# Optimization experiments

Measured on AMD Instinct MI355X. Metric: run time of the kernel, lower is better.

Reference implementation:

```python
import jax, jax.numpy as jnp
import numpy as np
from jax.scipy.ndimage import map_coordinates

IMG = 256
N_ANG = 50
BATCH = 4
N_CNN = 32
IN_CH = 2


def _circle_mask(S):
    c = (S - 1) / 2.0
    yy, xx = jnp.meshgrid(jnp.arange(S, dtype=jnp.float32), jnp.arange(S, dtype=jnp.float32), indexing='ij')
    return (((yy - c) ** 2 + (xx - c) ** 2) <= (S / 2.0) ** 2).astype(jnp.float32)


def radon_forward(img, angles):
    # img [B,1,S,S] -> sinogram [B,1,A,S]; parallel-beam, clip_to_circle=True
    S = img.shape[-1]
    c = (S - 1) / 2.0
    img = img * _circle_mask(S)
    t = jnp.arange(S, dtype=jnp.float32) - c        # integration coord
    s = jnp.arange(S, dtype=jnp.float32) - c        # detector coord
    cos = jnp.cos(angles)[:, None, None]
    sin = jnp.sin(angles)[:, None, None]
    x = s[None, None, :] * cos - t[None, :, None] * sin   # [A,S,S]
    y = s[None, None, :] * sin + t[None, :, None] * cos
    coords = jnp.stack([y + c, x + c])                    # [2,A,S,S] (row, col)
    samp = jax.vmap(lambda im: map_coordinates(im, coords, order=1, mode='constant', cval=0.0))(img[:, 0])  # [B,A,S,S]
    return samp.sum(axis=2)[:, None]                      # sum over ray param -> [B,1,A,S]


def filter_sinogram(sino):
    # Ram-Lak FFT filter with zero-padding + FBP normalization
    S = sino.shape[-1]
    A = sino.shape[2]
    P = max(64, int(2 ** np.ceil(np.log2(2 * S))))
    f = jnp.fft.rfft(jnp.pad(sino, ((0, 0), (0, 0), (0, 0), (0, P - S))), axis=-1)
    ramp = 2.0 * jnp.fft.rfftfreq(P).astype(jnp.float32)
    out = jnp.fft.irfft(f * ramp, n=P, axis=-1)[..., :S]
    return out * (np.pi / (2.0 * A))


def radon_backprojection(sino, angles):
    # sino [B,1,A,S] -> image [B,1,S,S]
    B, _, A, S = sino.shape
    c = (S - 1) / 2.0
    yy, xx = jnp.meshgrid(jnp.arange(S, dtype=jnp.float32) - c, jnp.arange(S, dtype=jnp.float32) - c, indexing='ij')
    cos = jnp.cos(angles)[:, None, None]
    sin = jnp.sin(angles)[:, None, None]
    det = xx[None] * cos + yy[None] * sin + c             # [A,S,S] detector coord
    sino2 = sino[:, 0]                                    # [B,A,S]

    def interp_one(sino_a, idx):
        # sino_a [B,S], idx [S,S] -> [B,S,S] linear interp, zero outside
        i0 = jnp.clip(jnp.floor(idx).astype(jnp.int32), 0, S - 2)
        w = idx - i0
        v = sino_a[:, i0] * (1.0 - w) + sino_a[:, i0 + 1] * w
        valid = (idx >= 0.0) & (idx <= S - 1.0)
        return jnp.where(valid, v, 0.0)

    bp = jax.vmap(interp_one, in_axes=(1, 0))(sino2, det).sum(axis=0)  # [B,S,S]
    return (bp * _circle_mask(S))[:, None]


def conv2d(x, w, b):
    y = jax.lax.conv_general_dilated(x, w, (1, 1), 'SAME', dimension_numbers=('NCHW', 'OIHW', 'NCHW'))
    return y + b[None, :, None, None]


def setup_inputs() -> dict:
    key = jax.random.key(0)
    ks = jax.random.split(key, 10)
    angles = jnp.asarray(np.linspace(0, np.pi, N_ANG, endpoint=False), dtype=jnp.float32)
    return {
        'x_sinogram': jax.random.normal(ks[0], (BATCH, 1, N_ANG, IMG), dtype=jnp.float32),
        'y_img_prev': jax.random.normal(ks[1], (BATCH, 1, IMG, IMG), dtype=jnp.float32),
        'y_img_concat_prev': jax.random.normal(ks[2], (BATCH, 1, IMG, IMG), dtype=jnp.float32),
        'angles': angles,
        'step': jnp.float32(1.0),
        'w1': jax.random.normal(ks[3], (N_CNN, IN_CH, 3, 3), dtype=jnp.float32) * 0.1,
        'b1': jnp.zeros((N_CNN,), dtype=jnp.float32),
        'w2': jax.random.normal(ks[4], (N_CNN, N_CNN, 3, 3), dtype=jnp.float32) * 0.1,
        'b2': jnp.zeros((N_CNN,), dtype=jnp.float32),
        'w3': jax.random.normal(ks[5], (1, N_CNN, 3, 3), dtype=jnp.float32) * 0.1,
        'b3': jnp.zeros((1,), dtype=jnp.float32),
    }


def reference(x_sinogram, y_img_prev, y_img_concat_prev, angles, step, w1, b1, w2, b2, w3, b3):
    Ay = radon_forward(y_img_prev, angles)                 # [B,1,A,S]
    diff = Ay - x_sinogram
    filt = filter_sinogram(diff)
    fbp = radon_backprojection(filt, angles)               # [B,1,S,S]
    y_img_update = y_img_prev + step * fbp
    y_cat = jnp.concatenate([y_img_update, y_img_concat_prev], axis=1)  # [B,2,S,S]
    h = jax.nn.relu(conv2d(y_cat, w1, b1))
    h = jax.nn.relu(conv2d(h, w2, b2))
    y_img = conv2d(h, w3, b3)
    return (y_img, y_img_update)
```

## Files before the change

### kernel.cpp

```cpp
#include <hip/hip_runtime.h>
#include <math.h>

#define IMGS 256
#define NANG 50
#define BATCH 4
#define NCNN 32
#define PIX (IMGS*IMGS)
#define NPIX (BATCH*PIX)

#define PROW 258
#define PPIX (PROW*PROW)
#define PB   (PPIX*NCNN)

#define OFF_FILT  0
#define OFF_W2BF  51200
#define OFF_H1P   55808

static constexpr double PI_D = 3.14159265358979323846;

typedef unsigned short u16;
typedef unsigned int   u32;
typedef unsigned long long u64;
typedef __bf16 bfrag __attribute__((ext_vector_type(8)));
typedef float  ffrag __attribute__((ext_vector_type(4)));

__device__ __forceinline__ u16 f2bf(float f) {
    u32 u = __float_as_uint(f);
    u += 0x7fffu + ((u >> 16) & 1u);
    return (u16)(u >> 16);
}

#define RPITCH_D 131
__global__ __launch_bounds__(1024, 4) void k_A(const float* __restrict__ angles,
                                               const float* __restrict__ yprev,
                                               const float* __restrict__ xsino,
                                               const float* __restrict__ w2,
                                               float* __restrict__ ws) {
    __shared__ u16 limg[258 * 262];
    __shared__ float spart[1024];
    __shared__ float staps[512];
    __shared__ float srow[256];
    int tid = threadIdx.x;
    int gid = blockIdx.x;
    if (gid >= 200) {
        int i = (gid - 200) * 1024 + tid;
        if (i < 9216) {
            int t = i >> 10, oc = (i >> 5) & 31, ic = i & 31;
            ((u16*)(ws + OFF_W2BF))[i] = f2bf(w2[(oc * 32 + ic) * 9 + t]);
        }
        return;
    }
    u32* l32 = (u32*)limg;
    int ra = gid;
    int a = ra % NANG, b = ra / NANG;

    if (tid < 511) {
        int d = tid - 255;
        int n = d < 0 ? -d : d;
        double g;
        if (n == 0) {
            g = 0.5;
        } else {
            double th = PI_D * (double)n / 256.0;
            double S = (256.0 * cos(255.0 * th) - 255.0 * cos(256.0 * th) - 1.0)
                       / (2.0 * (1.0 - cos(th)));
            double sign = (n & 1) ? -1.0 : 1.0;
            g = (sign + S / 128.0) / 512.0;
        }
        staps[tid] = (float)(g * PI_D / 100.0);
    }

    for (int z = tid; z < 772; z += 1024) {
        int addr;
        if (z < 258)      addr = z * RPITCH_D;
        else if (z < 516) addr = (z - 258) * RPITCH_D + 129;
        else if (z < 644) addr = (z - 516) + 1;
        else              addr = 257 * RPITCH_D + (z - 644) + 1;
        l32[addr] = 0;
    }
    const float* __restrict__ src = yprev + b * PIX;
    for (int idx = tid; idx < 16384; idx += 1024) {
        int r = idx >> 6, c4 = (idx & 63) << 2;
        float4 v = *(const float4*)(src + r * 256 + c4);
        float di = (float)r - 127.5f;
        float rr = di * di;
        float d0 = (float)c4 - 127.5f;
        v.x = (rr + d0 * d0 <= 16384.0f) ? v.x : 0.0f;
        v.y = (rr + (d0 + 1.0f) * (d0 + 1.0f) <= 16384.0f) ? v.y : 0.0f;
        v.z = (rr + (d0 + 2.0f) * (d0 + 2.0f) <= 16384.0f) ? v.z : 0.0f;
        v.w = (rr + (d0 + 3.0f) * (d0 + 3.0f) <= 16384.0f) ? v.w : 0.0f;
        u32 p0 = (u32)f2bf(v.x) | ((u32)f2bf(v.y) << 16);
        u32 p1 = (u32)f2bf(v.z) | ((u32)f2bf(v.w) << 16);
        int dw = (r + 1) * RPITCH_D + (c4 >> 1) + 1;
        l32[dw] = p0; l32[dw + 1] = p1;
    }
    __syncthreads();

    float a_ = angles[a];
    float cs = cosf(a_), sn = sinf(a_);
    int lane = tid & 63, w = tid >> 6;
    int s8 = lane & 7, t8 = lane >> 3;
    int sA = w * 16 + s8;
    float scA = (float)sA - 127.5f;
    float tc0 = (float)t8 - 127.5f;
    float rowA = scA * sn + tc0 * cs + 127.5f;
    float colA = scA * cs - tc0 * sn + 127.5f;
    float rowB = rowA + 8.0f * sn;
    float colB = colA + 8.0f * cs;
    float cs8 = 8.0f * cs, sn8 = 8.0f * sn;
    float accA = 0.0f, accB = 0.0f;
    #pragma unroll 4
    for (int j = 0; j < 32; ++j) {
        #pragma unroll
        for (int hh = 0; hh < 2; ++hh) {
            float rowv = hh ? rowB : rowA;
            float colv = hh ? colB : colA;
            float fr = floorf(rowv), fc = floorf(colv);
            float wr = rowv - fr, wc = colv - fc;
            int i0 = (int)fr, j0 = (int)fc;
            bool valid = (rowv > -1.0f) & (rowv < 256.0f) & (colv > -1.0f) & (colv < 256.0f);
            int i0c = min(max(i0, -1), 255);
            int j0c = min(max(j0, -1), 255);
            int ca = j0c + 2;
            int ka = ca >> 1;
            int sh = (ca & 1) << 4;
            int dw = (i0c + 1) * RPITCH_D + ka;
            u32 A = l32[dw],            C = l32[dw + 1];
            u32 B = l32[dw + RPITCH_D], D = l32[dw + RPITCH_D + 1];
            u32 top = (u32)((((u64)C << 32) | (u64)A) >> sh);
            u32 bot = (u32)((((u64)D << 32) | (u64)B) >> sh);
            float tl = __uint_as_float(top << 16);
            float tr_ = __uint_as_float(top & 0xffff0000u);
            float bl = __uint_as_float(bot << 16);
            float br = __uint_as_float(bot & 0xffff0000u);
            float tv = tl + (tr_ - tl) * wc;
            float bv = bl + (br - bl) * wc;
            float sv = tv + (bv - tv) * wr;
            sv = valid ? sv : 0.0f;
            if (hh) accB += sv; else accA += sv;
        }
        rowA += cs8; colA -= sn8; rowB += cs8; colB -= sn8;
    }
    accA += __shfl_xor(accA, 8, 64);
    accA += __shfl_xor(accA, 16, 64);
    accA += __shfl_xor(accA, 32, 64);
    accB += __shfl_xor(accB, 8, 64);
    accB += __shfl_xor(accB, 16, 64);
    accB += __shfl_xor(accB, 32, 64);
    if (t8 == 0) { spart[sA] = accA; spart[sA + 8] = accB; }
    __syncthreads();
    if (tid < 256)
        srow[tid] = spart[tid] - xsino[ra * 256 + tid];
    __syncthreads();
    {
        int s = tid & 255, q = tid >> 8;
        float fa = 0.0f;
        int m0 = q * 64;
        #pragma unroll 8
        for (int m = m0; m < m0 + 64; ++m) fa += srow[m] * staps[s - m + 255];
        spart[tid] = fa;
    }
    __syncthreads();
    if (tid < 256)
        ws[OFF_FILT + ra * 256 + tid] =
            spart[tid] + spart[tid + 256] + spart[tid + 512] + spart[tid + 768];
}

__global__ __launch_bounds__(512, 4) void k_B(const float* __restrict__ angles,
                                              const float* __restrict__ yprev,
                                              const float* __restrict__ yconc,
                                              const float* __restrict__ stepp,
                                              const float* __restrict__ w1,
                                              const float* __restrict__ b1,
                                              float* __restrict__ ws,
                                              float* __restrict__ dout) {
    __shared__ float sf[NANG * 256];
    __shared__ float supd[4][258];
    __shared__ float sy2[4][258];
    __shared__ float scs[NANG], ssn[NANG];
    int tid = threadIdx.x;
    int b = blockIdx.x >> 7, tile = blockIdx.x & 127;
    int y0 = tile << 1;

    {
        const float4* s4 = (const float4*)(ws + OFF_FILT + b * (NANG * 256));
        float4* d4 = (float4*)sf;
        for (int idx = tid; idx < NANG * 64; idx += 512) d4[idx] = s4[idx];
    }
    if (tid < NANG) {
        float a_ = angles[tid];
        scs[tid] = cosf(a_); ssn[tid] = sinf(a_);
    }
    if (tid < 8) supd[tid >> 1][(tid & 1) * 257] = 0.0f;
    for (int idx = tid; idx < 4 * 258; idx += 512) {
        int r = idx / 258, x = idx % 258;
        int iy = y0 - 1 + r, ix = x - 1;
        sy2[r][x] = ((unsigned)iy < 256u && (unsigned)ix < 256u)
                        ? yconc[b * PIX + iy * 256 + ix] : 0.0f;
    }
    if (tid < 144) {
        int px_i = tile * 9 + (tid >> 4), dw = tid & 15;
        if (px_i < 1028) {
            int y, x;
            if (px_i < 516) { y = (px_i < 258) ? 0 : 257; x = px_i % 258; }
            else            { int j = px_i - 516; y = 1 + (j >> 1); x = (j & 1) * 257; }
            u32* p = (u32*)((u16*)(ws + OFF_H1P) + b * PB + (y * PROW + x) * NCNN);
            p[dw] = 0;
        }
    }
    __syncthreads();

    float step = stepp[0];
    {
        int j = tid & 255, r0 = tid >> 8;
        float xx = (float)j - 127.5f;
        float yy0 = (float)(y0 - 1 + r0) - 127.5f;
        float acc[2] = {0.0f, 0.0f};
        #pragma unroll 5
        for (int a = 0; a < NANG; ++a) {
            float cs = scs[a], sn = ssn[a];
            float f0 = xx * cs + yy0 * sn + 127.5f;
            float idxf[2] = {f0, f0 + sn + sn};
            #pragma unroll
            for (int k = 0; k < 2; ++k) {
                float fl = floorf(idxf[k]);
                int i0 = (int)fl;
                i0 = min(max(i0, 0), 254);
                float w = idxf[k] - (float)i0;
                float v = sf[a * 256 + i0] * (1.0f - w) + sf[a * 256 + i0 + 1] * w;
                acc[k] += (idxf[k] >= 0.0f && idxf[k] <= 255.0f) ? v : 0.0f;
            }
        }
        #pragma unroll
        for (int k = 0; k < 2; ++k) {
            int r = r0 + 2 * k;
            int iy = y0 - 1 + r;
            float val = 0.0f;
            if ((unsigned)iy < 256u) {
                float yy = (float)iy - 127.5f;
                float m = (xx * xx + yy * yy <= 16384.0f) ? 1.0f : 0.0f;
                val = yprev[b * PIX + iy * 256 + j] + step * acc[k] * m;
                if (r >= 1 && r <= 2)
                    dout[NPIX + b * PIX + iy * 256 + j] = val;
            }
            supd[r][j + 1] = val;
        }
    }
    __syncthreads();

    {
        int wave = tid >> 6, lane = tid & 63;
        int oc0 = wave * 4;
        float W[72];
        const float4* wsrc = (const float4*)(w1 + oc0 * 18);
        #pragma unroll
        for (int i = 0; i < 18; ++i) ((float4*)W)[i] = wsrc[i];
        float bb0 = b1[oc0], bb1 = b1[oc0 + 1], bb2 = b1[oc0 + 2], bb3 = b1[oc0 + 3];
        u16* h1base = (u16*)(ws + OFF_H1P) + b * PB;
        #pragma unroll
        for (int it = 0; it < 8; ++it) {
            int px = it * 64 + lane;
            int rr = px >> 8, x = px & 255;
            int oy = y0 + rr;
            float v[18];
            #pragma unroll
            for (int ky = 0; ky < 3; ++ky)
                #pragma unroll
                for (int kx = 0; kx < 3; ++kx) {
                    v[ky * 3 + kx]     = supd[rr + ky][x + kx];
                    v[9 + ky * 3 + kx] = sy2[rr + ky][x + kx];
                }
            float a0 = bb0, a1 = bb1, a2 = bb2, a3 = bb3;
            #pragma unroll
            for (int t = 0; t < 18; ++t) {
                a0 += v[t] * W[t];
                a1 += v[t] * W[18 + t];
                a2 += v[t] * W[36 + t];
                a3 += v[t] * W[54 + t];
            }
            u32 p0 = (u32)f2bf(fmaxf(a0, 0.0f)) | ((u32)f2bf(fmaxf(a1, 0.0f)) << 16);
            u32 p1 = (u32)f2bf(fmaxf(a2, 0.0f)) | ((u32)f2bf(fmaxf(a3, 0.0f)) << 16);
            u32* op = (u32*)(h1base + ((oy + 1) * PROW + (x + 1)) * NCNN + oc0);
            op[0] = p0; op[1] = p1;
        }
    }
}

#define H2PITCH 34
__global__ __launch_bounds__(512, 4) void k_C(const float* __restrict__ b2,
                                              const float* __restrict__ w3,
                                              const float* __restrict__ b3,
                                              float* __restrict__ ws,
                                              float* __restrict__ dout) {
    __shared__ u16 sh2[4 * 258 * H2PITCH];
    __shared__ u32 swp[9 * 16];
    u32* l32 = (u32*)sh2;
    int tid = threadIdx.x;
    int b = blockIdx.x >> 7, tile = blockIdx.x & 127;
    int y0 = tile << 1;

    if (tid < 144) {
        int t = tid >> 4, kd = tid & 15;
        swp[tid] = (u32)f2bf(w3[(2 * kd) * 9 + t]) | ((u32)f2bf(w3[(2 * kd + 1) * 9 + t]) << 16);
    }
    if (tid < 136) {
        int r = tid / 34, rem = tid % 34;
        int col = (rem < 17) ? 0 : 257, dw = rem % 17;
        l32[(r * 258 + col) * 17 + dw] = 0;
    }
    #pragma unroll
    for (int r = 0; r < 4; ++r) {
        int hy = y0 - 1 + r;
        if (hy < 0 || hy > 255)
            for (int idx = tid; idx < 258 * 17; idx += 512)
                l32[r * 258 * 17 + idx] = 0;
    }
    __syncthreads();

    const u16* __restrict__ w2bf = (const u16*)(ws + OFF_W2BF);
    const u16* __restrict__ h1b  = (const u16*)(ws + OFF_H1P) + b * PB;
    int wave = tid >> 6, lane = tid & 63;
    int m = lane & 15, quad = lane >> 4;
    bfrag Bf[9][2];
    #pragma unroll
    for (int t = 0; t < 9; ++t) {
        const u16* wp = w2bf + t * 1024 + m * 32 + quad * 8;
        Bf[t][0] = *(const bfrag*)(wp);
        Bf[t][1] = *(const bfrag*)(wp + 16 * 32);
    }
    float bias0 = b2[m], bias1 = b2[m + 16];
    #pragma unroll
    for (int k = 0; k < 8; ++k) {
        int tl = wave + (k << 3);
        int ridx = tl >> 4, xt = tl & 15;
        int hy = y0 - 1 + ridx;
        bool valid = (unsigned)hy < 256u;
        int hyc = min(max(hy, 0), 255);
        int xs = xt << 4;
        bfrag A0[3], A1[3];
        #pragma unroll
        for (int tx = 0; tx < 3; ++tx)
            A0[tx] = *(const bfrag*)(h1b + ((hyc + 0) * PROW + xs + m + tx) * NCNN + quad * 8);
        #pragma unroll
        for (int tx = 0; tx < 3; ++tx)
            A1[tx] = *(const bfrag*)(h1b + ((hyc + 1) * PROW + xs + m + tx) * NCNN + quad * 8);
        ffrag c0 = {0.f, 0.f, 0.f, 0.f}, c1 = {0.f, 0.f, 0.f, 0.f};
        #pragma unroll
        for (int tx = 0; tx < 3; ++tx) {
            c0 = __builtin_amdgcn_mfma_f32_16x16x32_bf16(A0[tx], Bf[tx][0], c0, 0, 0, 0);
            c1 = __builtin_amdgcn_mfma_f32_16x16x32_bf16(A0[tx], Bf[tx][1], c1, 0, 0, 0);
        }
        #pragma unroll
        for (int tx = 0; tx < 3; ++tx)
            A0[tx] = *(const bfrag*)(h1b + ((hyc + 2) * PROW + xs + m + tx) * NCNN + quad * 8);
        #pragma unroll
        for (int tx = 0; tx < 3; ++tx) {
            c0 = __builtin_amdgcn_mfma_f32_16x16x32_bf16(A1[tx], Bf[3 + tx][0], c0, 0, 0, 0);
            c1 = __builtin_amdgcn_mfma_f32_16x16x32_bf16(A1[tx], Bf[3 + tx][1], c1, 0, 0, 0);
        }
        #pragma unroll
        for (int tx = 0; tx < 3; ++tx) {
            c0 = __builtin_amdgcn_mfma_f32_16x16x32_bf16(A0[tx], Bf[6 + tx][0], c0, 0, 0, 0);
            c1 = __builtin_amdgcn_mfma_f32_16x16x32_bf16(A0[tx], Bf[6 + tx][1], c1, 0, 0, 0);
        }
        if (valid) {
            #pragma unroll
            for (int r = 0; r < 4; ++r) {
                int px = xs + quad * 4 + r;
                u16* op = sh2 + (ridx * 258 + px + 1) * H2PITCH;
                op[m]      = f2bf(fmaxf(c0[r] + bias0, 0.0f));
                op[m + 16] = f2bf(fmaxf(c1[r] + bias1, 0.0f));
            }
        }
    }
    __syncthreads();

    {
        int rr = tid >> 8, x = tid & 255;
        int oy = y0 + rr;
        float acc = b3[0];
        #pragma unroll
        for (int ky = 0; ky < 3; ++ky) {
            #pragma unroll
            for (int cx = 0; cx < 3; ++cx) {
                int t = ky * 3 + cx;
                const u32* q = l32 + ((rr + ky) * 258 + x + cx) * 17;
                #pragma unroll
                for (int kd = 0; kd < 16; ++kd) {
                    u32 hv = q[kd];
                    u32 wv = swp[t * 16 + kd];
                    float h0 = __uint_as_float(hv << 16);
                    float h1 = __uint_as_float(hv & 0xffff0000u);
                    float w0 = __uint_as_float(wv << 16);
                    float w1_ = __uint_as_float(wv & 0xffff0000u);
                    acc += h0 * w0 + h1 * w1_;
                }
            }
        }
        dout[b * PIX + oy * 256 + x] = acc;
    }
}

extern "C" void kernel_launch(void* const* d_in, const int* in_sizes, int n_in,
                              void* d_out, int out_size, void* d_ws, size_t ws_size,
                              hipStream_t stream) {
    const float* xsino  = (const float*)d_in[0];
    const float* yprev  = (const float*)d_in[1];
    const float* yconc  = (const float*)d_in[2];
    const float* angles = (const float*)d_in[3];
    const float* stepp  = (const float*)d_in[4];
    const float* w1 = (const float*)d_in[5];
    const float* b1 = (const float*)d_in[6];
    const float* w2 = (const float*)d_in[7];
    const float* b2 = (const float*)d_in[8];
    const float* w3 = (const float*)d_in[9];
    const float* b3 = (const float*)d_in[10];
    float* out = (float*)d_out;
    float* ws  = (float*)d_ws;

    k_A<<<209, 1024, 0, stream>>>(angles, yprev, xsino, w2, ws);
    k_B<<<BATCH * 128, 512, 0, stream>>>(angles, yprev, yconc, stepp, w1, b1, ws, out);
    k_C<<<BATCH * 128, 512, 0, stream>>>(b2, w3, b3, ws, out);
}
```

Baseline: 154.7 us.

## Fuse three kernels into one cooperative kernel with grid syncs

Replaces the three separate launches (forward projection and filtering, backprojection with conv1, then conv2 and conv3) with a single cooperative kernel of 256 blocks of 1024 threads, using grid.sync between stages. Later stages loop over virtual tiles, and conv2 weights are converted to bf16 fragments in each block instead of being precomputed into the workspace. The aim is to remove kernel launch gaps and inter-kernel overhead. In exchange it adds two grid-wide barriers, runs the projection stage on only 200 of 256 blocks, and caps the grid at a size that must stay co-resident. Each block also redoes the weight conversion.

```diff
diff --git a/kernel.cpp b/kernel.cpp
--- a/kernel.cpp
+++ b/kernel.cpp
@@ -1,5 +1,8 @@
 #include <hip/hip_runtime.h>
+#include <hip/hip_cooperative_groups.h>
 #include <math.h>
+
+namespace cg = cooperative_groups;
 
 #define IMGS 256
 #define NANG 50
@@ -13,8 +16,7 @@
 #define PB   (PPIX*NCNN)
 
 #define OFF_FILT  0
-#define OFF_W2BF  51200
-#define OFF_H1P   55808
+#define OFF_H1P   51200
 
 static constexpr double PI_D = 3.14159265358979323846;
 
@@ -31,373 +33,368 @@
 }
 
 #define RPITCH_D 131
-__global__ __launch_bounds__(1024, 4) void k_A(const float* __restrict__ angles,
-                                               const float* __restrict__ yprev,
-                                               const float* __restrict__ xsino,
-                                               const float* __restrict__ w2,
-                                               float* __restrict__ ws) {
-    __shared__ u16 limg[258 * 262];
-    __shared__ float spart[1024];
-    __shared__ float staps[512];
-    __shared__ float srow[256];
-    int tid = threadIdx.x;
-    int gid = blockIdx.x;
-    if (gid >= 200) {
-        int i = (gid - 200) * 1024 + tid;
-        if (i < 9216) {
-            int t = i >> 10, oc = (i >> 5) & 31, ic = i & 31;
-            ((u16*)(ws + OFF_W2BF))[i] = f2bf(w2[(oc * 32 + ic) * 9 + t]);
-        }
-        return;
+#define H2PITCH 34
+
+__global__ __launch_bounds__(1024, 4) void k_fused(
+    const float* __restrict__ xsino, const float* __restrict__ yprev,
+    const float* __restrict__ yconc, const float* __restrict__ angles,
+    const float* __restrict__ stepp, const float* __restrict__ w1,
+    const float* __restrict__ b1, const float* __restrict__ w2,
+    const float* __restrict__ b2, const float* __restrict__ w3,
+    const float* __restrict__ b3, float* __restrict__ ws,
+    float* __restrict__ dout)
+{
+    __shared__ __align__(16) char smem[142400];
+    cg::grid_group grid = cg::this_grid();
+    int tid = threadIdx.x, bid = blockIdx.x;
+
+    if (bid < 200) {
+        u16* limg   = (u16*)smem;
+        u32* l32    = (u32*)smem;
+        float* spart = (float*)(smem + 135232);
+        float* staps = (float*)(smem + 139328);
+        float* srow  = (float*)(smem + 141376);
+        int ra = bid;
+        int a = ra % NANG, b = ra / NANG;
+
+        if (tid < 511) {
+            int d = tid - 255;
+            int n = d < 0 ? -d : d;
+            double g;
+            if (n == 0) {
+                g = 0.5;
+            } else {
+                double th = PI_D * (double)n / 256.0;
+                double S = (256.0 * cos(255.0 * th) - 255.0 * cos(256.0 * th) - 1.0)
+                           / (2.0 * (1.0 - cos(th)));
+                double sign = (n & 1) ? -1.0 : 1.0;
+                g = (sign + S / 128.0) / 512.0;
+            }
+            staps[tid] = (float)(g * PI_D / 100.0);
+        }
+        for (int z = tid; z < 772; z += 1024) {
+            int addr;
+            if (z < 258)      addr = z * RPITCH_D;
+            else if (z < 516) addr = (z - 258) * RPITCH_D + 129;
+            else if (z < 644) addr = (z - 516) + 1;
+            else              addr = 257 * RPITCH_D + (z - 644) + 1;
+            l32[addr] = 0;
+        }
+        const float* __restrict__ src = yprev + b * PIX;
+        for (int idx = tid; idx < 16384; idx += 1024) {
+            int r = idx >> 6, c4 = (idx & 63) << 2;
+            float4 v = *(const float4*)(src + r * 256 + c4);
+            float di = (float)r - 127.5f;
+            float rr = di * di;
+            float d0 = (float)c4 - 127.5f;
+            v.x = (rr + d0 * d0 <= 16384.0f) ? v.x : 0.0f;
+            v.y = (rr + (d0 + 1.0f) * (d0 + 1.0f) <= 16384.0f) ? v.y : 0.0f;
+            v.z = (rr + (d0 + 2.0f) * (d0 + 2.0f) <= 16384.0f) ? v.z : 0.0f;
+            v.w = (rr + (d0 + 3.0f) * (d0 + 3.0f) <= 16384.0f) ? v.w : 0.0f;
+            u32 p0 = (u32)f2bf(v.x) | ((u32)f2bf(v.y) << 16);
+            u32 p1 = (u32)f2bf(v.z) | ((u32)f2bf(v.w) << 16);
+            int dw = (r + 1) * RPITCH_D + (c4 >> 1) + 1;
+            l32[dw] = p0; l32[dw + 1] = p1;
+        }
+        __syncthreads();
+
+        float a_ = angles[a];
+        float cs = cosf(a_), sn = sinf(a_);
+        int lane = tid & 63, wv_ = tid >> 6;
+        int s8 = lane & 7, t8 = lane >> 3;
+        int sA = wv_ * 16 + s8;
+        float scA = (float)sA - 127.5f;
+        float tc0 = (float)t8 - 127.5f;
+        float rowA = scA * sn + tc0 * cs + 127.5f;
+        float colA = scA * cs - tc0 * sn + 127.5f;
+        float rowB = rowA + 8.0f * sn;
+        float colB = colA + 8.0f * cs;
+        float cs8 = 8.0f * cs, sn8 = 8.0f * sn;
+        float accA = 0.0f, accB = 0.0f;
+        #pragma unroll 4
+        for (int j = 0; j < 32; ++j) {
+            #pragma unroll
+            for (int hh = 0; hh < 2; ++hh) {
+                float rowv = hh ? rowB : rowA;
+                float colv = hh ? colB : colA;
+                float fr = floorf(rowv), fc = floorf(colv);
+                float wr = rowv - fr, wc = colv - fc;
+                int i0 = (int)fr, j0 = (int)fc;
+                bool valid = (rowv > -1.0f) & (rowv < 256.0f) & (colv > -1.0f) & (colv < 256.0f);
+                int i0c = min(max(i0, -1), 255);
+                int j0c = min(max(j0, -1), 255);
+                int ca = j0c + 2;
+                int ka = ca >> 1;
+                int sh = (ca & 1) << 4;
+                int dw = (i0c + 1) * RPITCH_D + ka;
+                u32 A = l32[dw],            C = l32[dw + 1];
+                u32 B = l32[dw + RPITCH_D], D = l32[dw + RPITCH_D + 1];
+                u32 top = (u32)((((u64)C << 32) | (u64)A) >> sh);
+                u32 bot = (u32)((((u64)D << 32) | (u64)B) >> sh);
+                float tl = __uint_as_float(top << 16);
+                float tr_ = __uint_as_float(top & 0xffff0000u);
+                float bl = __uint_as_float(bot << 16);
+                float br = __uint_as_float(bot & 0xffff0000u);
+                float tv = tl + (tr_ - tl) * wc;
+                float bv = bl + (br - bl) * wc;
+                float sv = tv + (bv - tv) * wr;
+                sv = valid ? sv : 0.0f;
+                if (hh) accB += sv; else accA += sv;
+            }
+            rowA += cs8; colA -= sn8; rowB += cs8; colB -= sn8;
+        }
+        accA += __shfl_xor(accA, 8, 64);
+        accA += __shfl_xor(accA, 16, 64);
+        accA += __shfl_xor(accA, 32, 64);
+        accB += __shfl_xor(accB, 8, 64);
+        accB += __shfl_xor(accB, 16, 64);
+        accB += __shfl_xor(accB, 32, 64);
+        if (t8 == 0) { spart[sA] = accA; spart[sA + 8] = accB; }
+        __syncthreads();
+        if (tid < 256)
+            srow[tid] = spart[tid] - xsino[ra * 256 + tid];
+        __syncthreads();
+        {
+            int s = tid & 255, q = tid >> 8;
+            float fa = 0.0f;
+            int m0 = q * 64;
+            #pragma unroll 8
+            for (int m = m0; m < m0 + 64; ++m) fa += srow[m] * staps[s - m + 255];
+            spart[tid] = fa;
+        }
+        __syncthreads();
+        if (tid < 256)
+            ws[OFF_FILT + ra * 256 + tid] =
+                spart[tid] + spart[tid + 256] + spart[tid + 512] + spart[tid + 768];
     }
-    u32* l32 = (u32*)limg;
-    int ra = gid;
-    int a = ra % NANG, b = ra / NANG;
-
-    if (tid < 511) {
-        int d = tid - 255;
-        int n = d < 0 ? -d : d;
-        double g;
-        if (n == 0) {
-            g = 0.5;
-        } else {
-            double th = PI_D * (double)n / 256.0;
-            double S = (256.0 * cos(255.0 * th) - 255.0 * cos(256.0 * th) - 1.0)
-                       / (2.0 * (1.0 - cos(th)));
-            double sign = (n & 1) ? -1.0 : 1.0;
-            g = (sign + S / 128.0) / 512.0;
-        }
-        staps[tid] = (float)(g * PI_D / 100.0);
+    __threadfence();
+    grid.sync();
+
+    {
+        float* sf          = (float*)smem;
+        float (*supd)[258] = (float(*)[258])(smem + 51200);
+        float (*sy2)[258]  = (float(*)[258])(smem + 55328);
+        float* scs         = (float*)(smem + 59456);
+        float* ssn         = (float*)(smem + 59656);
+        float step = stepp[0];
+        for (int vt = bid; vt < 512; vt += 256) {
+            int b = vt >> 7, tile = vt & 127, y0 = tile << 1;
+            {
+                const float4* s4 = (const float4*)(ws + OFF_FILT + b * (NANG * 256));
+                float4* d4 = (float4*)sf;
+                for (int idx = tid; idx < NANG * 64; idx += 1024) d4[idx] = s4[idx];
+            }
+            if (tid < NANG) {
+                float a_ = angles[tid];
+                scs[tid] = cosf(a_); ssn[tid] = sinf(a_);
+            }
+            if (tid < 8) supd[tid >> 1][(tid & 1) * 257] = 0.0f;
+            for (int idx = tid; idx < 4 * 258; idx += 1024) {
+                int r = idx / 258, x = idx % 258;
+                int iy = y0 - 1 + r, ix = x - 1;
+                sy2[r][x] = ((unsigned)iy < 256u && (unsigned)ix < 256u)
+                                ? yconc[b * PIX + iy * 256 + ix] : 0.0f;
+            }
+            if (tid < 144) {
+                int px_i = tile * 9 + (tid >> 4), dw = tid & 15;
+                if (px_i < 1028) {
+                    int y, x;
+                    if (px_i < 516) { y = (px_i < 258) ? 0 : 257; x = px_i % 258; }
+                    else            { int j = px_i - 516; y = 1 + (j >> 1); x = (j & 1) * 257; }
+                    u32* p = (u32*)((u16*)(ws + OFF_H1P) + b * PB + (y * PROW + x) * NCNN);
+                    p[dw] = 0;
+                }
+            }
+            __syncthreads();
+
+            {
+                int r = tid >> 8, j = tid & 255;
+                int iy = y0 - 1 + r;
+                float val = 0.0f;
+                if ((unsigned)iy < 256u) {
+                    float yy = (float)iy - 127.5f, xx = (float)j - 127.5f;
+                    float acc = 0.0f;
+                    #pragma unroll 5
+                    for (int a = 0; a < NANG; ++a) {
+                        float idxf = xx * scs[a] + yy * ssn[a] + 127.5f;
+                        float fl = floorf(idxf);
+                        int i0 = (int)fl;
+                        i0 = min(max(i0, 0), 254);
+                        float w = idxf - (float)i0;
+                        float v = sf[a * 256 + i0] * (1.0f - w) + sf[a * 256 + i0 + 1] * w;
+                        acc += (idxf >= 0.0f && idxf <= 255.0f) ? v : 0.0f;
+                    }
+                    float m = (xx * xx + yy * yy <= 16384.0f) ? 1.0f : 0.0f;
+                    val = yprev[b * PIX + iy * 256 + j] + step * acc * m;
+                    if (r == 1 || r == 2)
+                        dout[NPIX + b * PIX + iy * 256 + j] = val;
+                }
+                supd[r][j + 1] = val;
+            }
+            __syncthreads();
+
+            {
+                int wave = tid >> 6, lane = tid & 63;
+                int row = wave >> 3, oc0 = (wave & 7) * 4;
+                int oy = y0 + row;
+                float W[72];
+                const float4* wsrc = (const float4*)(w1 + oc0 * 18);
+                #pragma unroll
+                for (int i = 0; i < 18; ++i) ((float4*)W)[i] = wsrc[i];
+                float bb0 = b1[oc0], bb1 = b1[oc0 + 1], bb2 = b1[oc0 + 2], bb3 = b1[oc0 + 3];
+                u16* h1base = (u16*)(ws + OFF_H1P) + b * PB;
+                #pragma unroll
+                for (int it = 0; it < 4; ++it) {
+                    int x = it * 64 + lane;
+                    float v[18];
+                    #pragma unroll
+                    for (int ky = 0; ky < 3; ++ky)
+                        #pragma unroll
+                        for (int kx = 0; kx < 3; ++kx) {
+                            v[ky * 3 + kx]     = supd[row + ky][x + kx];
+                            v[9 + ky * 3 + kx] = sy2[row + ky][x + kx];
+                        }
+                    float a0 = bb0, a1 = bb1, a2 = bb2, a3 = bb3;
+                    #pragma unroll
+                    for (int t = 0; t < 18; ++t) {
+                        a0 += v[t] * W[t];
+                        a1 += v[t] * W[18 + t];
+                        a2 += v[t] * W[36 + t];
+                        a3 += v[t] * W[54 + t];
+                    }
+                    u32 p0 = (u32)f2bf(fmaxf(a0, 0.0f)) | ((u32)f2bf(fmaxf(a1, 0.0f)) << 16);
+                    u32 p1 = (u32)f2bf(fmaxf(a2, 0.0f)) | ((u32)f2bf(fmaxf(a3, 0.0f)) << 16);
+                    u32* op = (u32*)(h1base + ((oy + 1) * PROW + (x + 1)) * NCNN + oc0);
+                    op[0] = p0; op[1] = p1;
+                }
+            }
+            __syncthreads();
+        }
     }
-
-    for (int z = tid; z < 772; z += 1024) {
-        int addr;
-        if (z < 258)      addr = z * RPITCH_D;
-        else if (z < 516) addr = (z - 258) * RPITCH_D + 129;
-        else if (z < 644) addr = (z - 516) + 1;
-        else              addr = 257 * RPITCH_D + (z - 644) + 1;
-        l32[addr] = 0;
-    }
-    const float* __restrict__ src = yprev + b * PIX;
-    for (int idx = tid; idx < 16384; idx += 1024) {
-        int r = idx >> 6, c4 = (idx & 63) << 2;
-        float4 v = *(const float4*)(src + r * 256 + c4);
-        float di = (float)r - 127.5f;
-        float rr = di * di;
-        float d0 = (float)c4 - 127.5f;
-        v.x = (rr + d0 * d0 <= 16384.0f) ? v.x : 0.0f;
-        v.y = (rr + (d0 + 1.0f) * (d0 + 1.0f) <= 16384.0f) ? v.y : 0.0f;
-        v.z = (rr + (d0 + 2.0f) * (d0 + 2.0f) <= 16384.0f) ? v.z : 0.0f;
-        v.w = (rr + (d0 + 3.0f) * (d0 + 3.0f) <= 16384.0f) ? v.w : 0.0f;
-        u32 p0 = (u32)f2bf(v.x) | ((u32)f2bf(v.y) << 16);
-        u32 p1 = (u32)f2bf(v.z) | ((u32)f2bf(v.w) << 16);
-        int dw = (r + 1) * RPITCH_D + (c4 >> 1) + 1;
-        l32[dw] = p0; l32[dw + 1] = p1;
-    }
-    __syncthreads();
-
-    float a_ = angles[a];
-    float cs = cosf(a_), sn = sinf(a_);
-    int lane = tid & 63, w = tid >> 6;
-    int s8 = lane & 7, t8 = lane >> 3;
-    int sA = w * 16 + s8;
-    float scA = (float)sA - 127.5f;
-    float tc0 = (float)t8 - 127.5f;
-    float rowA = scA * sn + tc0 * cs + 127.5f;
-    float colA = scA * cs - tc0 * sn + 127.5f;
-    float rowB = rowA + 8.0f * sn;
-    float colB = colA + 8.0f * cs;
-    float cs8 = 8.0f * cs, sn8 = 8.0f * sn;
-    float accA = 0.0f, accB = 0.0f;
-    #pragma unroll 4
-    for (int j = 0; j < 32; ++j) {
+    __threadfence();
+    grid.sync();
+
+    {
+        u16* sh2 = (u16*)smem;
+        u32* l32 = (u32*)smem;
+        u32* swp = (u32*)(smem + 70176);
+        const u16* __restrict__ h1p = (const u16*)(ws + OFF_H1P);
+        int wave = tid >> 6, lane = tid & 63;
+        int m = lane & 15, quad = lane >> 4;
+        bfrag Bf[9][2];
         #pragma unroll
-        for (int hh = 0; hh < 2; ++hh) {
-            float rowv = hh ? rowB : rowA;
-            float colv = hh ? colB : colA;
-            float fr = floorf(rowv), fc = floorf(colv);
-            float wr = rowv - fr, wc = colv - fc;
-            int i0 = (int)fr, j0 = (int)fc;
-            bool valid = (rowv > -1.0f) & (rowv < 256.0f) & (colv > -1.0f) & (colv < 256.0f);
-            int i0c = min(max(i0, -1), 255);
-            int j0c = min(max(j0, -1), 255);
-            int ca = j0c + 2;
-            int ka = ca >> 1;
-            int sh = (ca & 1) << 4;
-            int dw = (i0c + 1) * RPITCH_D + ka;
-            u32 A = l32[dw],            C = l32[dw + 1];
-            u32 B = l32[dw + RPITCH_D], D = l32[dw + RPITCH_D + 1];
-            u32 top = (u32)((((u64)C << 32) | (u64)A) >> sh);
-            u32 bot = (u32)((((u64)D << 32) | (u64)B) >> sh);
-            float tl = __uint_as_float(top << 16);
-            float tr_ = __uint_as_float(top & 0xffff0000u);
-            float bl = __uint_as_float(bot << 16);
-            float br = __uint_as_float(bot & 0xffff0000u);
-            float tv = tl + (tr_ - tl) * wc;
-            float bv = bl + (br - bl) * wc;
-            float sv = tv + (bv - tv) * wr;
-            sv = valid ? sv : 0.0f;
-            if (hh) accB += sv; else accA += sv;
-        }
-        rowA += cs8; colA -= sn8; rowB += cs8; colB -= sn8;
-    }
-    accA += __shfl_xor(accA, 8, 64);
-    accA += __shfl_xor(accA, 16, 64);
-    accA += __shfl_xor(accA, 32, 64);
-    accB += __shfl_xor(accB, 8, 64);
-    accB += __shfl_xor(accB, 16, 64);
-    accB += __shfl_xor(accB, 32, 64);
-    if (t8 == 0) { spart[sA] = accA; spart[sA + 8] = accB; }
-    __syncthreads();
-    if (tid < 256)
-        srow[tid] = spart[tid] - xsino[ra * 256 + tid];
-    __syncthreads();
-    {
-        int s = tid & 255, q = tid >> 8;
-        float fa = 0.0f;
-        int m0 = q * 64;
-        #pragma unroll 8
-        for (int m = m0; m < m0 + 64; ++m) fa += srow[m] * staps[s - m + 255];
-        spart[tid] = fa;
-    }
-    __syncthreads();
-    if (tid < 256)
-        ws[OFF_FILT + ra * 256 + tid] =
-            spart[tid] + spart[tid + 256] + spart[tid + 512] + spart[tid + 768];
-}
-
-__global__ __launch_bounds__(512, 4) void k_B(const float* __restrict__ angles,
-                                              const float* __restrict__ yprev,
-                                              const float* __restrict__ yconc,
-                                              const float* __restrict__ stepp,
-                                              const float* __restrict__ w1,
-                                              const float* __restrict__ b1,
-                                              float* __restrict__ ws,
-                                              float* __restrict__ dout) {
-    __shared__ float sf[NANG * 256];
-    __shared__ float supd[4][258];
-    __shared__ float sy2[4][258];
-    __shared__ float scs[NANG], ssn[NANG];
-    int tid = threadIdx.x;
-    int b = blockIdx.x >> 7, tile = blockIdx.x & 127;
-    int y0 = tile << 1;
-
-    {
-        const float4* s4 = (const float4*)(ws + OFF_FILT + b * (NANG * 256));
-        float4* d4 = (float4*)sf;
-        for (int idx = tid; idx < NANG * 64; idx += 512) d4[idx] = s4[idx];
-    }
-    if (tid < NANG) {
-        float a_ = angles[tid];
-        scs[tid] = cosf(a_); ssn[tid] = sinf(a_);
-    }
-    if (tid < 8) supd[tid >> 1][(tid & 1) * 257] = 0.0f;
-    for (int idx = tid; idx < 4 * 258; idx += 512) {
-        int r = idx / 258, x = idx % 258;
-        int iy = y0 - 1 + r, ix = x - 1;
-        sy2[r][x] = ((unsigned)iy < 256u && (unsigned)ix < 256u)
-                        ? yconc[b * PIX + iy * 256 + ix] : 0.0f;
-    }
-    if (tid < 144) {
-        int px_i = tile * 9 + (tid >> 4), dw = tid & 15;
-        if (px_i < 1028) {
-            int y, x;
-            if (px_i < 516) { y = (px_i < 258) ? 0 : 257; x = px_i % 258; }
-            else            { int j = px_i - 516; y = 1 + (j >> 1); x = (j & 1) * 257; }
-            u32* p = (u32*)((u16*)(ws + OFF_H1P) + b * PB + (y * PROW + x) * NCNN);
-            p[dw] = 0;
-        }
-    }
-    __syncthreads();
-
-    float step = stepp[0];
-    {
-        int j = tid & 255, r0 = tid >> 8;
-        float xx = (float)j - 127.5f;
-        float yy0 = (float)(y0 - 1 + r0) - 127.5f;
-        float acc[2] = {0.0f, 0.0f};
-        #pragma unroll 5
-        for (int a = 0; a < NANG; ++a) {
-            float cs = scs[a], sn = ssn[a];
-            float f0 = xx * cs + yy0 * sn + 127.5f;
-            float idxf[2] = {f0, f0 + sn + sn};
+        for (int t = 0; t < 9; ++t) {
             #pragma unroll
-            for (int k = 0; k < 2; ++k) {
-                float fl = floorf(idxf[k]);
-                int i0 = (int)fl;
-                i0 = min(max(i0, 0), 254);
-                float w = idxf[k] - (float)i0;
-                float v = sf[a * 256 + i0] * (1.0f - w) + sf[a * 256 + i0 + 1] * w;
-                acc[k] += (idxf[k] >= 0.0f && idxf[k] <= 255.0f) ? v : 0.0f;
-            }
-        }
-        #pragma unroll
-        for (int k = 0; k < 2; ++k) {
-            int r = r0 + 2 * k;
-            int iy = y0 - 1 + r;
-            float val = 0.0f;
-            if ((unsigned)iy < 256u) {
-                float yy = (float)iy - 127.5f;
-                float m = (xx * xx + yy * yy <= 16384.0f) ? 1.0f : 0.0f;
-                val = yprev[b * PIX + iy * 256 + j] + step * acc[k] * m;
-                if (r >= 1 && r <= 2)
-                    dout[NPIX + b * PIX + iy * 256 + j] = val;
-            }
-            supd[r][j + 1] = val;
-        }
-    }
-    __syncthreads();
-
-    {
-        int wave = tid >> 6, lane = tid & 63;
-        int oc0 = wave * 4;
-        float W[72];
-        const float4* wsrc = (const float4*)(w1 + oc0 * 18);
-        #pragma unroll
-        for (int i = 0; i < 18; ++i) ((float4*)W)[i] = wsrc[i];
-        float bb0 = b1[oc0], bb1 = b1[oc0 + 1], bb2 = b1[oc0 + 2], bb3 = b1[oc0 + 3];
-        u16* h1base = (u16*)(ws + OFF_H1P) + b * PB;
-        #pragma unroll
-        for (int it = 0; it < 8; ++it) {
-            int px = it * 64 + lane;
-            int rr = px >> 8, x = px & 255;
-            int oy = y0 + rr;
-            float v[18];
-            #pragma unroll
-            for (int ky = 0; ky < 3; ++ky)
-                #pragma unroll
-                for (int kx = 0; kx < 3; ++kx) {
-                    v[ky * 3 + kx]     = supd[rr + ky][x + kx];
-                    v[9 + ky * 3 + kx] = sy2[rr + ky][x + kx];
-                }
-            float a0 = bb0, a1 = bb1, a2 = bb2, a3 = bb3;
-            #pragma unroll
-            for (int t = 0; t < 18; ++t) {
-                a0 += v[t] * W[t];
-                a1 += v[t] * W[18 + t];
-                a2 += v[t] * W[36 + t];
-                a3 += v[t] * W[54 + t];
-            }
-            u32 p0 = (u32)f2bf(fmaxf(a0, 0.0f)) | ((u32)f2bf(fmaxf(a1, 0.0f)) << 16);
-            u32 p1 = (u32)f2bf(fmaxf(a2, 0.0f)) | ((u32)f2bf(fmaxf(a3, 0.0f)) << 16);
-            u32* op = (u32*)(h1base + ((oy + 1) * PROW + (x + 1)) * NCNN + oc0);
-            op[0] = p0; op[1] = p1;
-        }
-    }
-}
-
-#define H2PITCH 34
-__global__ __launch_bounds__(512, 4) void k_C(const float* __restrict__ b2,
-                                              const float* __restrict__ w3,
-                                              const float* __restrict__ b3,
-                                              float* __restrict__ ws,
-                                              float* __restrict__ dout) {
-    __shared__ u16 sh2[4 * 258 * H2PITCH];
-    __shared__ u32 swp[9 * 16];
-    u32* l32 = (u32*)sh2;
-    int tid = threadIdx.x;
-    int b = blockIdx.x >> 7, tile = blockIdx.x & 127;
-    int y0 = tile << 1;
-
-    if (tid < 144) {
-        int t = tid >> 4, kd = tid & 15;
-        swp[tid] = (u32)f2bf(w3[(2 * kd) * 9 + t]) | ((u32)f2bf(w3[(2 * kd + 1) * 9 + t]) << 16);
-    }
-    if (tid < 136) {
-        int r = tid / 34, rem = tid % 34;
-        int col = (rem < 17) ? 0 : 257, dw = rem % 17;
-        l32[(r * 258 + col) * 17 + dw] = 0;
-    }
-    #pragma unroll
-    for (int r = 0; r < 4; ++r) {
-        int hy = y0 - 1 + r;
-        if (hy < 0 || hy > 255)
-            for (int idx = tid; idx < 258 * 17; idx += 512)
-                l32[r * 258 * 17 + idx] = 0;
-    }
-    __syncthreads();
-
-    const u16* __restrict__ w2bf = (const u16*)(ws + OFF_W2BF);
-    const u16* __restrict__ h1b  = (const u16*)(ws + OFF_H1P) + b * PB;
-    int wave = tid >> 6, lane = tid & 63;
-    int m = lane & 15, quad = lane >> 4;
-    bfrag Bf[9][2];
-    #pragma unroll
-    for (int t = 0; t < 9; ++t) {
-        const u16* wp = w2bf + t * 1024 + m * 32 + quad * 8;
-        Bf[t][0] = *(const bfrag*)(wp);
-        Bf[t][1] = *(const bfrag*)(wp + 16 * 32);
-    }
-    float bias0 = b2[m], bias1 = b2[m + 16];
-    #pragma unroll
-    for (int k = 0; k < 8; ++k) {
-        int tl = wave + (k << 3);
-        int ridx = tl >> 4, xt = tl & 15;
-        int hy = y0 - 1 + ridx;
-        bool valid = (unsigned)hy < 256u;
-        int hyc = min(max(hy, 0), 255);
-        int xs = xt << 4;
-        bfrag A0[3], A1[3];
-        #pragma unroll
-        for (int tx = 0; tx < 3; ++tx)
-            A0[tx] = *(const bfrag*)(h1b + ((hyc + 0) * PROW + xs + m + tx) * NCNN + quad * 8);
-        #pragma unroll
-        for (int tx = 0; tx < 3; ++tx)
-            A1[tx] = *(const bfrag*)(h1b + ((hyc + 1) * PROW + xs + m + tx) * NCNN + quad * 8);
-        ffrag c0 = {0.f, 0.f, 0.f, 0.f}, c1 = {0.f, 0.f, 0.f, 0.f};
-        #pragma unroll
-        for (int tx = 0; tx < 3; ++tx) {
-            c0 = __builtin_amdgcn_mfma_f32_16x16x32_bf16(A0[tx], Bf[tx][0], c0, 0, 0, 0);
-            c1 = __builtin_amdgcn_mfma_f32_16x16x32_bf16(A0[tx], Bf[tx][1], c1, 0, 0, 0);
-        }
-        #pragma unroll
-        for (int tx = 0; tx < 3; ++tx)
-            A0[tx] = *(const bfrag*)(h1b + ((hyc + 2) * PROW + xs + m + tx) * NCNN + quad * 8);
-        #pragma unroll
-        for (int tx = 0; tx < 3; ++tx) {
-            c0 = __builtin_amdgcn_mfma_f32_16x16x32_bf16(A1[tx], Bf[3 + tx][0], c0, 0, 0, 0);
-            c1 = __builtin_amdgcn_mfma_f32_16x16x32_bf16(A1[tx], Bf[3 + tx][1], c1, 0, 0, 0);
-        }
-        #pragma unroll
-        for (int tx = 0; tx < 3; ++tx) {
-            c0 = __builtin_amdgcn_mfma_f32_16x16x32_bf16(A0[tx], Bf[6 + tx][0], c0, 0, 0, 0);
-            c1 = __builtin_amdgcn_mfma_f32_16x16x32_bf16(A0[tx], Bf[6 + tx][1], c1, 0, 0, 0);
-        }
-        if (valid) {
+            for (int h = 0; h < 2; ++h) {
+                int oc = m + 16 * h;
+                bfrag f;
+                #pragma unroll
+                for (int jj = 0; jj < 8; ++jj) {
+                    int ic = quad * 8 + jj;
+                    u16 bv = f2bf(w2[(oc * 32 + ic) * 9 + t]);
+                    f[jj] = *(__bf16*)&bv;
+                }
+                Bf[t][h] = f;
+            }
+        }
+        float bias0 = b2[m], bias1 = b2[m + 16];
+        for (int vt = bid; vt < 512; vt += 256) {
+            int b = vt >> 7, tile = vt & 127, y0 = tile << 1;
+            if (tid < 144) {
+                int t = tid >> 4, kd = tid & 15;
+                swp[tid] = (u32)f2bf(w3[(2 * kd) * 9 + t]) | ((u32)f2bf(w3[(2 * kd + 1) * 9 + t]) << 16);
+            }
+            if (tid < 136) {
+                int r = tid / 34, rem = tid % 34;
+                int col = (rem < 17) ? 0 : 257, dw = rem % 17;
+                l32[(r * 258 + col) * 17 + dw] = 0;
+            }
             #pragma unroll
             for (int r = 0; r < 4; ++r) {
-                int px = xs + quad * 4 + r;
-                u16* op = sh2 + (ridx * 258 + px + 1) * H2PITCH;
-                op[m]      = f2bf(fmaxf(c0[r] + bias0, 0.0f));
-                op[m + 16] = f2bf(fmaxf(c1[r] + bias1, 0.0f));
-            }
-        }
-    }
-    __syncthreads();
-
-    {
-        int rr = tid >> 8, x = tid & 255;
-        int oy = y0 + rr;
-        float acc = b3[0];
-        #pragma unroll
-        for (int ky = 0; ky < 3; ++ky) {
+                int hy = y0 - 1 + r;
+                if (hy < 0 || hy > 255)
+                    for (int idx = tid; idx < 258 * 17; idx += 1024)
+                        l32[r * 258 * 17 + idx] = 0;
+            }
+            __syncthreads();
+
+            const u16* __restrict__ h1b = h1p + b * PB;
             #pragma unroll
-            for (int cx = 0; cx < 3; ++cx) {
-                int t = ky * 3 + cx;
-                const u32* q = l32 + ((rr + ky) * 258 + x + cx) * 17;
-                #pragma unroll
-                for (int kd = 0; kd < 16; ++kd) {
-                    u32 hv = q[kd];
-                    u32 wv = swp[t * 16 + kd];
-                    float h0 = __uint_as_float(hv << 16);
-                    float h1 = __uint_as_float(hv & 0xffff0000u);
-                    float w0 = __uint_as_float(wv << 16);
-                    float w1_ = __uint_as_float(wv & 0xffff0000u);
-                    acc += h0 * w0 + h1 * w1_;
-                }
-            }
-        }
-        dout[b * PIX + oy * 256 + x] = acc;
+            for (int k = 0; k < 4; ++k) {
+                int tl = wave + (k << 4);
+                int ridx = tl >> 4, xt = tl & 15;
+                int hy = y0 - 1 + ridx;
+                bool valid = (unsigned)hy < 256u;
+                int hyc = min(max(hy, 0), 255);
+                int xs = xt << 4;
+                bfrag A0[3], A1[3];
+                #pragma unroll
+                for (int tx = 0; tx < 3; ++tx)
+                    A0[tx] = *(const bfrag*)(h1b + ((hyc + 0) * PROW + xs + m + tx) * NCNN + quad * 8);
+                #pragma unroll
+                for (int tx = 0; tx < 3; ++tx)
+                    A1[tx] = *(const bfrag*)(h1b + ((hyc + 1) * PROW + xs + m + tx) * NCNN + quad * 8);
+                ffrag c0 = {0.f, 0.f, 0.f, 0.f}, c1 = {0.f, 0.f, 0.f, 0.f};
+                #pragma unroll
+                for (int tx = 0; tx < 3; ++tx) {
+                    c0 = __builtin_amdgcn_mfma_f32_16x16x32_bf16(A0[tx], Bf[tx][0], c0, 0, 0, 0);
+                    c1 = __builtin_amdgcn_mfma_f32_16x16x32_bf16(A0[tx], Bf[tx][1], c1, 0, 0, 0);
+                }
+                #pragma unroll
+                for (int tx = 0; tx < 3; ++tx)
+                    A0[tx] = *(const bfrag*)(h1b + ((hyc + 2) * PROW + xs + m + tx) * NCNN + quad * 8);
+                #pragma unroll
+                for (int tx = 0; tx < 3; ++tx) {
+                    c0 = __builtin_amdgcn_mfma_f32_16x16x32_bf16(A1[tx], Bf[3 + tx][0], c0, 0, 0, 0);
+                    c1 = __builtin_amdgcn_mfma_f32_16x16x32_bf16(A1[tx], Bf[3 + tx][1], c1, 0, 0, 0);
+                }
+                #pragma unroll
+                for (int tx = 0; tx < 3; ++tx) {
+                    c0 = __builtin_amdgcn_mfma_f32_16x16x32_bf16(A0[tx], Bf[6 + tx][0], c0, 0, 0, 0);
+                    c1 = __builtin_amdgcn_mfma_f32_16x16x32_bf16(A0[tx], Bf[6 + tx][1], c1, 0, 0, 0);
+                }
+                if (valid) {
+                    #pragma unroll
+                    for (int r = 0; r < 4; ++r) {
+                        int px = xs + quad * 4 + r;
+                        u16* op = sh2 + (ridx * 258 + px + 1) * H2PITCH;
+                        op[m]      = f2bf(fmaxf(c0[r] + bias0, 0.0f));
+                        op[m + 16] = f2bf(fmaxf(c1[r] + bias1, 0.0f));
+                    }
+                }
+            }
+            __syncthreads();
+
+            {
+                int px = tid >> 1, half = tid & 1;
+                int rr = px >> 8, x = px & 255;
+                int oy = y0 + rr;
+                float acc = 0.0f;
+                #pragma unroll
+                for (int ky = 0; ky < 3; ++ky) {
+                    #pragma unroll
+                    for (int cx = 0; cx < 3; ++cx) {
+                        int t = ky * 3 + cx;
+                        const u32* q = l32 + ((rr + ky) * 258 + x + cx) * 17 + half * 8;
+                        const u32* wq = swp + t * 16 + half * 8;
+                        #pragma unroll
+                        for (int kd = 0; kd < 8; ++kd) {
+                            u32 hv = q[kd];
+                            u32 wvv = wq[kd];
+                            float h0 = __uint_as_float(hv << 16);
+                            float h1 = __uint_as_float(hv & 0xffff0000u);
+                            float w0 = __uint_as_float(wvv << 16);
+                            float w1_ = __uint_as_float(wvv & 0xffff0000u);
+                            acc += h0 * w0 + h1 * w1_;
+                        }
+                    }
+                }
+                acc += __shfl_xor(acc, 1, 64);
+                if (half == 0)
+                    dout[b * PIX + oy * 256 + x] = acc + b3[0];
+            }
+            __syncthreads();
+        }
     }
 }
 
@@ -418,7 +415,9 @@
     float* out = (float*)d_out;
     float* ws  = (float*)d_ws;
 
-    k_A<<<209, 1024, 0, stream>>>(angles, yprev, xsino, w2, ws);
-    k_B<<<BATCH * 128, 512, 0, stream>>>(angles, yprev, yconc, stepp, w1, b1, ws, out);
-    k_C<<<BATCH * 128, 512, 0, stream>>>(b2, w3, b3, ws, out);
+    void* args[] = {(void*)&xsino, (void*)&yprev, (void*)&yconc, (void*)&angles,
+                    (void*)&stepp, (void*)&w1, (void*)&b1, (void*)&w2, (void*)&b2,
+                    (void*)&w3, (void*)&b3, (void*)&ws, (void*)&out};
+    hipLaunchCooperativeKernel((const void*)k_fused, dim3(256), dim3(1024),
+                               args, 0, stream);
 }
```

Measured after the change: 436.2 us. 182% more time.
